# Performance work log

Measured on AMD Instinct MI355X. Metric: run time of the kernel, lower is better.

## Reference

```python
import jax, jax.numpy as jnp
import numpy as np

B, J, D = 1024, 17, 512          # batch, joints, encoder hidden dim
M, K, DT = 34, 2048, 512         # tokens per pose, codebook size, token dim
DDEC, DDEC_I = 32, 64            # decoder hidden dims
L_ENC, L_DEC = 4, 1
DECAY = 0.9
EPS = 1e-5


def _ln(x, g, b):
    m = jnp.mean(x, -1, keepdims=True)
    v = jnp.mean((x - m) ** 2, -1, keepdims=True)
    return (x - m) * jax.lax.rsqrt(v + EPS) * g + b


def _mlp(x, w1, b1, w2, b2):
    return jax.nn.gelu(x @ w1 + b1, approximate=False) @ w2 + b2


def _mixer(x, p, i):
    ln1g, ln1b, tw1, tb1, tw2, tb2, ln2g, ln2b, cw1, cb1, cw2, cb2 = (a[i] for a in p)
    y = jnp.swapaxes(_ln(x, ln1g, ln1b), 1, 2)        # token-mixing over joints
    y = jnp.swapaxes(_mlp(y, tw1, tb1, tw2, tb2), 1, 2)
    z = _mlp(_ln(x + y, ln2g, ln2b), cw1, cb1, cw2, cb2)  # channel-mixing
    return x + y + z


def _forward(joints, invisible_token, start_w, start_b,
             enc_ln1_g, enc_ln1_b, enc_tw1, enc_tb1, enc_tw2, enc_tb2,
             enc_ln2_g, enc_ln2_b, enc_cw1, enc_cb1, enc_cw2, enc_cb2,
             enc_ln_g, enc_ln_b, token_mlp_w, token_mlp_b, feat_w, feat_b,
             dec_ln1_g, dec_ln1_b, dec_tw1, dec_tb1, dec_tw2, dec_tb2,
             dec_ln2_g, dec_ln2_b, dec_cw1, dec_cb1, dec_cw2, dec_cb2,
             dec_token_mlp_w, dec_token_mlp_b, dec_start_w, dec_start_b,
             dec_ln_g, dec_ln_b, rec_w, rec_b,
             codebook, ema_cluster_size, ema_w):
    x = joints[:, :, :2] @ start_w + start_b                  # [B,J,D]
    vis = (joints[:, :, 2:] != 0).astype(x.dtype)             # [B,J,1]
    x = x * vis + invisible_token * (1.0 - vis)
    encp = (enc_ln1_g, enc_ln1_b, enc_tw1, enc_tb1, enc_tw2, enc_tb2,
            enc_ln2_g, enc_ln2_b, enc_cw1, enc_cb1, enc_cw2, enc_cb2)
    for i in range(L_ENC):
        x = _mixer(x, encp, i)
    x = _ln(x, enc_ln_g, enc_ln_b)
    # token_mlp: Linear over joints axis: [B,D,J] -> [B,D,M] -> [B,M,D]
    x = jnp.einsum('bjd,jm->bmd', x, token_mlp_w) + token_mlp_b[None, :, None]
    feat = (x @ feat_w + feat_b).reshape(B * M, DT)           # encode_feat [N,DT]
    # squared euclidean distances to codebook entries
    dists = (jnp.sum(feat * feat, 1, keepdims=True)
             + jnp.sum(codebook * codebook, 1)
             - 2.0 * feat @ codebook.T)                       # [N,K]
    idx = jnp.argmin(dists, axis=1)                           # [N]
    quant = codebook[idx]                                     # == one_hot(idx) @ codebook
    # EMA codebook update (buffers; single-device so all_reduce == identity)
    sg_feat = jax.lax.stop_gradient(feat)
    counts = jax.ops.segment_sum(jnp.ones((B * M,), feat.dtype), idx, num_segments=K)
    dw = jax.ops.segment_sum(sg_feat, idx, num_segments=K)    # == encodings.T @ feat
    cs = ema_cluster_size * DECAY + (1.0 - DECAY) * counts
    n = jnp.sum(cs)
    cs = (cs + 1e-5) / (n + K * 1e-5) * n                     # laplace smoothing
    ema_w_new = ema_w * DECAY + (1.0 - DECAY) * dw
    codebook_new = ema_w_new / cs[:, None]
    e_latent_loss = jnp.mean(jnp.square(jax.lax.stop_gradient(quant) - feat))
    quant = feat + jax.lax.stop_gradient(quant - feat)        # straight-through
    ptf = quant.reshape(B, M, DT)
    out_ptf = jax.lax.stop_gradient(ptf)
    # decoder_token_mlp: Linear over token axis: [B,DT,M] -> [B,DT,J] -> [B,J,DT]
    y = jnp.einsum('bmd,mj->bjd', ptf, dec_token_mlp_w) + dec_token_mlp_b[None, :, None]
    y = y @ dec_start_w + dec_start_b                         # [B,J,DDEC]
    decp = (dec_ln1_g, dec_ln1_b, dec_tw1, dec_tb1, dec_tw2, dec_tb2,
            dec_ln2_g, dec_ln2_b, dec_cw1, dec_cb1, dec_cw2, dec_cb2)
    for i in range(L_DEC):
        y = _mixer(y, decp, i)
    y = _ln(y, dec_ln_g, dec_ln_b)
    rec = y @ rec_w + rec_b                                   # [B,J,2]
    return rec, idx, e_latent_loss, out_ptf, codebook_new


def setup_inputs():
    ks = iter(jax.random.split(jax.random.key(0), 64))
    def nrm(shape, s=0.02):
        return jax.random.normal(next(ks), shape, jnp.float32) * s
    inp = {}
    coords = jax.random.uniform(next(ks), (B, J, 2), jnp.float32)
    inp['joints'] = jnp.concatenate([coords, jnp.ones((B, J, 1), jnp.float32)], -1)
    inp['joints_feature'] = nrm((B, J, 256), 1.0)   # unused (guide_ratio=0)
    inp['cls_logits'] = jnp.zeros((1, 1), jnp.float32)  # unused in tokenizer stage
    inp['invisible_token'] = nrm((1, 1, D))
    inp['start_w'], inp['start_b'] = nrm((2, D)), jnp.zeros((D,), jnp.float32)
    for pre, L, H, HI in (('enc', L_ENC, D, D), ('dec', L_DEC, DDEC, DDEC_I)):
        inp[pre + '_ln1_g'], inp[pre + '_ln1_b'] = jnp.ones((L, H)), jnp.zeros((L, H))
        inp[pre + '_tw1'], inp[pre + '_tb1'] = nrm((L, J, 64)), jnp.zeros((L, 64))
        inp[pre + '_tw2'], inp[pre + '_tb2'] = nrm((L, 64, J)), jnp.zeros((L, J))
        inp[pre + '_ln2_g'], inp[pre + '_ln2_b'] = jnp.ones((L, H)), jnp.zeros((L, H))
        inp[pre + '_cw1'], inp[pre + '_cb1'] = nrm((L, H, HI)), jnp.zeros((L, HI))
        inp[pre + '_cw2'], inp[pre + '_cb2'] = nrm((L, HI, H)), jnp.zeros((L, H))
    inp['enc_ln_g'], inp['enc_ln_b'] = jnp.ones((D,)), jnp.zeros((D,))
    inp['token_mlp_w'], inp['token_mlp_b'] = nrm((J, M)), jnp.zeros((M,))
    inp['feat_w'], inp['feat_b'] = nrm((D, DT)), jnp.zeros((DT,))
    inp['codebook'] = jax.random.normal(next(ks), (K, DT), jnp.float32)
    inp['ema_cluster_size'] = jnp.zeros((K,), jnp.float32)
    inp['ema_w'] = jax.random.normal(next(ks), (K, DT), jnp.float32)
    inp['dec_token_mlp_w'], inp['dec_token_mlp_b'] = nrm((M, J)), jnp.zeros((J,))
    inp['dec_start_w'], inp['dec_start_b'] = nrm((DT, DDEC)), jnp.zeros((DDEC,))
    inp['dec_ln_g'], inp['dec_ln_b'] = jnp.ones((DDEC,)), jnp.zeros((DDEC,))
    inp['rec_w'], inp['rec_b'] = nrm((DDEC, 2)), jnp.zeros((2,))
    return inp


def reference(joints, joints_feature, cls_logits, invisible_token, start_w, start_b,
              enc_ln1_g, enc_ln1_b, enc_tw1, enc_tb1, enc_tw2, enc_tb2,
              enc_ln2_g, enc_ln2_b, enc_cw1, enc_cb1, enc_cw2, enc_cb2,
              enc_ln_g, enc_ln_b, token_mlp_w, token_mlp_b, feat_w, feat_b,
              codebook, ema_cluster_size, ema_w,
              dec_ln1_g, dec_ln1_b, dec_tw1, dec_tb1, dec_tw2, dec_tb2,
              dec_ln2_g, dec_ln2_b, dec_cw1, dec_cb1, dec_cw2, dec_cb2,
              dec_token_mlp_w, dec_token_mlp_b, dec_start_w, dec_start_b,
              dec_ln_g, dec_ln_b, rec_w, rec_b):
    # joints_feature / cls_logits unused: guide_ratio=0, stage_pct='tokenizer'
    return _forward(joints, invisible_token, start_w, start_b,
                    enc_ln1_g, enc_ln1_b, enc_tw1, enc_tb1, enc_tw2, enc_tb2,
                    enc_ln2_g, enc_ln2_b, enc_cw1, enc_cb1, enc_cw2, enc_cb2,
                    enc_ln_g, enc_ln_b, token_mlp_w, token_mlp_b, feat_w, feat_b,
                    dec_ln1_g, dec_ln1_b, dec_tw1, dec_tb1, dec_tw2, dec_tb2,
                    dec_ln2_g, dec_ln2_b, dec_cw1, dec_cb1, dec_cw2, dec_cb2,
                    dec_token_mlp_w, dec_token_mlp_b, dec_start_w, dec_start_b,
                    dec_ln_g, dec_ln_b, rec_w, rec_b,
                    codebook, ema_cluster_size, ema_w)
```

## Files before the change

### kernel.cpp

```cpp
#include <hip/hip_runtime.h>
#include <math.h>

constexpr int Bn = 1024, Jn = 17, Mn = 34;
constexpr int RJ = Bn * Jn;
constexpr int RM = Bn * Mn;
constexpr size_t SZX = (size_t)RJ * 512;
constexpr size_t SZM = (size_t)RM * 512;

typedef __attribute__((ext_vector_type(8))) short bf16x8;
typedef __attribute__((ext_vector_type(4))) float f32x4;
typedef unsigned long long u64;
typedef unsigned short u16;
typedef unsigned int u32;

__device__ __forceinline__ float gelu_f(float x) {
  return 0.5f * x * (1.0f + erff(x * 0.7071067811865475f));
}
__device__ __forceinline__ u16 bf16_rne(float x) {
  u32 u = __float_as_uint(x);
  u += 0x7fffu + ((u >> 16) & 1u);
  return (u16)(u >> 16);
}
__device__ __forceinline__ float bf16_f(u16 h) {
  return __uint_as_float((u32)h << 16);
}

typedef __attribute__((address_space(1))) const void gas_t;
typedef __attribute__((address_space(3))) void las_t;
__device__ __forceinline__ void gll16(const void* g, void* l) {
  __builtin_amdgcn_global_load_lds((gas_t*)g, (las_t*)l, 16, 0, 0);
}

__global__ __launch_bounds__(256) void embed_kernel(
    const float* __restrict__ joints, const float* __restrict__ inv,
    const float* __restrict__ sw, const float* __restrict__ sb,
    float* __restrict__ out) {
  int tid = blockIdx.x * 256 + threadIdx.x;
  int row = tid >> 9, d = tid & 511;
  float j0 = joints[row * 3 + 0];
  float j1 = joints[row * 3 + 1];
  float j2 = joints[row * 3 + 2];
  float x = fmaf(j0, sw[d], fmaf(j1, sw[512 + d], sb[d]));
  float v = (j2 != 0.0f) ? 1.0f : 0.0f;
  out[tid] = x * v + inv[d] * (1.0f - v);
}

__global__ __launch_bounds__(256) void mixer_fused(
    const float* __restrict__ x_in, float* __restrict__ res_out,
    u16* __restrict__ oh, u16* __restrict__ ol,
    const float* __restrict__ g1, const float* __restrict__ b1,
    const float* __restrict__ tw1, const float* __restrict__ tb1,
    const float* __restrict__ tw2, const float* __restrict__ tb2,
    const float* __restrict__ g2, const float* __restrict__ b2,
    const float* __restrict__ W1, const float* __restrict__ W2,
    u16* __restrict__ Th1, u16* __restrict__ Tl1,
    u16* __restrict__ Th2, u16* __restrict__ Tl2) {
  __shared__ float xs[17][512];
  __shared__ float sw1[17 * 64], sw2[64 * 17], sb1v[64], sb2v[17];
  __shared__ float stats[17][2];
  const int tid = threadIdx.x;
  const int b = blockIdx.x;
  {
    int gid = b * 256 + tid;
    int k = gid >> 9, n = gid & 511;
    float v = W1[gid];
    u16 h = bf16_rne(v);
    Th1[(size_t)n * 512 + k] = h;
    Tl1[(size_t)n * 512 + k] = bf16_rne(v - bf16_f(h));
    v = W2[gid];
    h = bf16_rne(v);
    Th2[(size_t)n * 512 + k] = h;
    Tl2[(size_t)n * 512 + k] = bf16_rne(v - bf16_f(h));
  }
  for (int i = tid; i < 17 * 64; i += 256) { sw1[i] = tw1[i]; sw2[i] = tw2[i]; }
  if (tid < 64) sb1v[tid] = tb1[tid];
  if (tid < 17) sb2v[tid] = tb2[tid];
  const float* px = x_in + (size_t)b * 17 * 512;
  for (int i = tid; i < 17 * 512; i += 256) xs[i >> 9][i & 511] = px[i];
  __syncthreads();
  const int wv = tid >> 6, ln_ = tid & 63;
  for (int j = wv; j < 17; j += 4) {
    float v[8];
    float s = 0.0f;
#pragma unroll
    for (int i = 0; i < 8; i++) { v[i] = xs[j][ln_ + 64 * i]; s += v[i]; }
#pragma unroll
    for (int m = 32; m; m >>= 1) s += __shfl_xor(s, m);
    float mean = s * (1.0f / 512.0f);
    float s2 = 0.0f;
#pragma unroll
    for (int i = 0; i < 8; i++) { float t = v[i] - mean; s2 += t * t; }
#pragma unroll
    for (int m = 32; m; m >>= 1) s2 += __shfl_xor(s2, m);
    float rs = 1.0f / sqrtf(s2 * (1.0f / 512.0f) + 1e-5f);
    if (ln_ == 0) { stats[j][0] = mean; stats[j][1] = rs; }
  }
  __syncthreads();
  for (int cc = 0; cc < 2; cc++) {
    int d = tid + cc * 256;
    float gd = g1[d], bd = b1[d];
    float t[17], acc[17];
#pragma unroll
    for (int j = 0; j < 17; j++) {
      t[j] = (xs[j][d] - stats[j][0]) * stats[j][1] * gd + bd;
      acc[j] = 0.0f;
    }
    for (int k = 0; k < 64; k++) {
      float h = sb1v[k];
#pragma unroll
      for (int j = 0; j < 17; j++) h = fmaf(t[j], sw1[j * 64 + k], h);
      h = gelu_f(h);
#pragma unroll
      for (int j = 0; j < 17; j++) acc[j] = fmaf(h, sw2[k * 17 + j], acc[j]);
    }
#pragma unroll
    for (int j = 0; j < 17; j++) {
      float r = xs[j][d] + acc[j] + sb2v[j];
      xs[j][d] = r;
      res_out[((size_t)b * 17 + j) * 512 + d] = r;
    }
  }
  __syncthreads();
  for (int j = wv; j < 17; j += 4) {
    float v[8];
    float s = 0.0f;
#pragma unroll
    for (int i = 0; i < 8; i++) { v[i] = xs[j][ln_ + 64 * i]; s += v[i]; }
#pragma unroll
    for (int m = 32; m; m >>= 1) s += __shfl_xor(s, m);
    float mean = s * (1.0f / 512.0f);
    float s2 = 0.0f;
#pragma unroll
    for (int i = 0; i < 8; i++) { float t = v[i] - mean; s2 += t * t; }
#pragma unroll
    for (int m = 32; m; m >>= 1) s2 += __shfl_xor(s2, m);
    float rs = 1.0f / sqrtf(s2 * (1.0f / 512.0f) + 1e-5f);
#pragma unroll
    for (int i = 0; i < 8; i++) {
      int d = ln_ + 64 * i;
      float o = (v[i] - mean) * rs * g2[d] + b2[d];
      u16 h = bf16_rne(o);
      size_t off = ((size_t)b * 17 + j) * 512 + d;
      oh[off] = h;
      ol[off] = bf16_rne(o - bf16_f(h));
    }
  }
}

__global__ __launch_bounds__(256) void lnmix_fused(
    const float* __restrict__ x_in, u16* __restrict__ oh, u16* __restrict__ ol,
    const float* __restrict__ g, const float* __restrict__ bb,
    const float* __restrict__ w, const float* __restrict__ bias,
    const float* __restrict__ Wf, u16* __restrict__ Thf, u16* __restrict__ Tlf) {
  __shared__ float xs[17][513];
  __shared__ float sw[17 * 34], sb[34];
  const int tid = threadIdx.x;
  const int b = blockIdx.x;
  {
    int gid = b * 256 + tid;
    int k = gid >> 9, n = gid & 511;
    float v = Wf[gid];
    u16 h = bf16_rne(v);
    Thf[(size_t)n * 512 + k] = h;
    Tlf[(size_t)n * 512 + k] = bf16_rne(v - bf16_f(h));
  }
  for (int i = tid; i < 17 * 34; i += 256) sw[i] = w[i];
  if (tid < 34) sb[tid] = bias[tid];
  const float* px = x_in + (size_t)b * 17 * 512;
  for (int i = tid; i < 17 * 512; i += 256) xs[i >> 9][i & 511] = px[i];
  __syncthreads();
  const int wv = tid >> 6, ln_ = tid & 63;
  for (int j = wv; j < 17; j += 4) {
    float v[8];
    float s = 0.0f;
#pragma unroll
    for (int i = 0; i < 8; i++) { v[i] = xs[j][ln_ + 64 * i]; s += v[i]; }
#pragma unroll
    for (int m = 32; m; m >>= 1) s += __shfl_xor(s, m);
    float mean = s * (1.0f / 512.0f);
    float s2 = 0.0f;
#pragma unroll
    for (int i = 0; i < 8; i++) { float t = v[i] - mean; s2 += t * t; }
#pragma unroll
    for (int m = 32; m; m >>= 1) s2 += __shfl_xor(s2, m);
    float rs = 1.0f / sqrtf(s2 * (1.0f / 512.0f) + 1e-5f);
#pragma unroll
    for (int i = 0; i < 8; i++) {
      int d = ln_ + 64 * i;
      xs[j][d] = (v[i] - mean) * rs * g[d] + bb[d];
    }
  }
  __syncthreads();
  for (int cc = 0; cc < 2; cc++) {
    int d = tid + cc * 256;
    float t[17];
#pragma unroll
    for (int j = 0; j < 17; j++) t[j] = xs[j][d];
#pragma unroll
    for (int m = 0; m < 34; m++) {
      float s = sb[m];
#pragma unroll
      for (int j = 0; j < 17; j++) s = fmaf(t[j], sw[j * 34 + m], s);
      size_t o = ((size_t)b * 34 + m) * 512 + d;
      u16 h = bf16_rne(s);
      oh[o] = h;
      ol[o] = bf16_rne(s - bf16_f(h));
    }
  }
}

__global__ __launch_bounds__(256) void splitnorm_kernel(
    const float* __restrict__ CBm, u16* __restrict__ hi, u16* __restrict__ lo,
    float* __restrict__ cnorm, u64* __restrict__ packed, int* __restrict__ cnt) {
  int gid = blockIdx.x * 256 + threadIdx.x;
  for (int i = gid; i < RM; i += 131072) packed[i] = ~0ull;
  if (gid < 2048) cnt[gid] = 0;
  int wave = threadIdx.x >> 6, lane = threadIdx.x & 63;
  int k = blockIdx.x * 4 + wave;
  const float4* p4 = (const float4*)(CBm + (size_t)k * 512);
  ushort4* h4 = (ushort4*)(hi + (size_t)k * 512);
  ushort4* l4 = (ushort4*)(lo + (size_t)k * 512);
  float s = 0.0f;
#pragma unroll
  for (int i = 0; i < 2; i++) {
    float4 x = p4[lane + 64 * i];
    ushort4 h, l;
    h.x = bf16_rne(x.x); l.x = bf16_rne(x.x - bf16_f(h.x));
    h.y = bf16_rne(x.y); l.y = bf16_rne(x.y - bf16_f(h.y));
    h.z = bf16_rne(x.z); l.z = bf16_rne(x.z - bf16_f(h.z));
    h.w = bf16_rne(x.w); l.w = bf16_rne(x.w - bf16_f(h.w));
    h4[lane + 64 * i] = h;
    l4[lane + 64 * i] = l;
    s = fmaf(x.x, x.x, s); s = fmaf(x.y, x.y, s);
    s = fmaf(x.z, x.z, s); s = fmaf(x.w, x.w, s);
  }
#pragma unroll
  for (int m = 32; m; m >>= 1) s += __shfl_xor(s, m);
  if (lane == 0) cnorm[k] = s;
}

template <int GELU_FLAG, int RES_FLAG, int HILO_OUT>
__global__ __launch_bounds__(256, 4) void mgemm64(
    const u16* __restrict__ Ah, const u16* __restrict__ Al,
    const u16* __restrict__ Bh, const u16* __restrict__ Bl,
    const float* __restrict__ bias, const float* __restrict__ R,
    float* __restrict__ C, u16* __restrict__ Oh, u16* __restrict__ Ol, int N) {
  __shared__ __align__(16) u16 sAh[2048], sAl[2048], sBh[4096], sBl[4096];
  const int tid = threadIdx.x;
  const int m0 = blockIdx.x * 64, n0 = blockIdx.y * 128;
  const int lane = tid & 63, wave = tid >> 6;
  const int wm = wave >> 1, wn = wave & 1;
  const int fr = lane & 15, q = lane >> 4;
  const int ra = tid >> 2, ca = (tid & 3) ^ ((ra >> 1) & 3);
  const size_t aoff = (size_t)(m0 + ra) * 512 + ca * 8;
  const int rb0 = tid >> 2, cb0 = (tid & 3) ^ ((rb0 >> 1) & 3);
  const int ci1 = tid + 256;
  const int rb1 = ci1 >> 2, cb1 = (ci1 & 3) ^ ((rb1 >> 1) & 3);
  const size_t boff0 = (size_t)(n0 + rb0) * 512 + cb0 * 8;
  const size_t boff1 = (size_t)(n0 + rb1) * 512 + cb1 * 8;
  const int ldA = wave * 512;
  const int ldB0 = wave * 512, ldB1 = 2048 + wave * 512;
  int fca[2], fcb[4];
#pragma unroll
  for (int mt = 0; mt < 2; mt++) {
    int rra = wm * 32 + mt * 16 + fr;
    fca[mt] = (rra * 4 + (q ^ ((rra >> 1) & 3))) * 8;
  }
#pragma unroll
  for (int nt = 0; nt < 4; nt++) {
    int rrb = wn * 64 + nt * 16 + fr;
    fcb[nt] = (rrb * 4 + (q ^ ((rrb >> 1) & 3))) * 8;
  }
  f32x4 acc[2][4];
#pragma unroll
  for (int i = 0; i < 2; i++)
#pragma unroll
    for (int j = 0; j < 4; j++) {
      acc[i][j][0] = 0.0f; acc[i][j][1] = 0.0f;
      acc[i][j][2] = 0.0f; acc[i][j][3] = 0.0f;
    }
  for (int k0 = 0; k0 < 512; k0 += 32) {
    gll16(Ah + aoff + k0, &sAh[ldA]);
    gll16(Al + aoff + k0, &sAl[ldA]);
    gll16(Bh + boff0 + k0, &sBh[ldB0]);
    gll16(Bh + boff1 + k0, &sBh[ldB1]);
    gll16(Bl + boff0 + k0, &sBl[ldB0]);
    gll16(Bl + boff1 + k0, &sBl[ldB1]);
    __syncthreads();
    bf16x8 fah[2], fal[2], fbh[4], fbl[4];
#pragma unroll
    for (int mt = 0; mt < 2; mt++) {
      fah[mt] = *(const bf16x8*)&sAh[fca[mt]];
      fal[mt] = *(const bf16x8*)&sAl[fca[mt]];
    }
#pragma unroll
    for (int nt = 0; nt < 4; nt++) {
      fbh[nt] = *(const bf16x8*)&sBh[fcb[nt]];
      fbl[nt] = *(const bf16x8*)&sBl[fcb[nt]];
    }
#pragma unroll
    for (int mt = 0; mt < 2; mt++)
#pragma unroll
      for (int nt = 0; nt < 4; nt++) {
        acc[mt][nt] = __builtin_amdgcn_mfma_f32_16x16x32_bf16(
            fah[mt], fbh[nt], acc[mt][nt], 0, 0, 0);
        acc[mt][nt] = __builtin_amdgcn_mfma_f32_16x16x32_bf16(
            fah[mt], fbl[nt], acc[mt][nt], 0, 0, 0);
        acc[mt][nt] = __builtin_amdgcn_mfma_f32_16x16x32_bf16(
            fal[mt], fbh[nt], acc[mt][nt], 0, 0, 0);
      }
    __syncthreads();
  }
#pragma unroll
  for (int mt = 0; mt < 2; mt++)
#pragma unroll
    for (int reg = 0; reg < 4; reg++) {
      int row = m0 + wm * 32 + mt * 16 + q * 4 + reg;
#pragma unroll
      for (int nt = 0; nt < 4; nt++) {
        int col = n0 + wn * 64 + nt * 16 + fr;
        float v = acc[mt][nt][reg] + bias[col];
        if (GELU_FLAG) v = gelu_f(v);
        if (RES_FLAG) v += R[(size_t)row * N + col];
        if (HILO_OUT) {
          u16 h = bf16_rne(v);
          Oh[(size_t)row * N + col] = h;
          Ol[(size_t)row * N + col] = bf16_rne(v - bf16_f(h));
        } else {
          C[(size_t)row * N + col] = v;
        }
      }
    }
}

#define MG_PROLOGUE()                                                        \
  const int tid = threadIdx.x;                                               \
  const int m0 = blockIdx.x * 128, n0 = blockIdx.y * 128;                    \
  const int lane = tid & 63, wave = tid >> 6;                                \
  const int wm = wave >> 1, wn = wave & 1;                                   \
  const int fr = lane & 15, q = lane >> 4, qd = q;                           \
  const int ci0 = wave * 128 + lane, ci1 = ci0 + 64;                         \
  const int r0 = ci0 >> 2, c0x = (ci0 & 3) ^ ((r0 >> 1) & 3);                \
  const int r1 = ci1 >> 2, c1x = (ci1 & 3) ^ ((r1 >> 1) & 3);                \
  const size_t aoff0 = (size_t)(m0 + r0) * 512 + c0x * 8;                    \
  const size_t aoff1 = (size_t)(m0 + r1) * 512 + c1x * 8;                    \
  const size_t boff0 = (size_t)(n0 + r0) * 512 + c0x * 8;                    \
  const size_t boff1 = (size_t)(n0 + r1) * 512 + c1x * 8;                    \
  const int ld0 = wave * 1024, ld1 = ld0 + 512;       \
  int fca[4], fcb[4];                                                        \
  _Pragma("unroll") for (int t4 = 0; t4 < 4; t4++) {                         \
    int rra = wm * 64 + t4 * 16 + fr;                                        \
    int rrb = wn * 64 + t4 * 16 + fr;                                        \
    int sz = q ^ ((fr >> 1) & 3);                                            \
    fca[t4] = (rra * 4 + sz) * 8;                                            \
    fcb[t4] = (rrb * 4 + sz) * 8;                                            \
  }                                                                          \
  f32x4 acc[4][4];                                                           \
  _Pragma("unroll") for (int i = 0; i < 4; i++)                              \
    _Pragma("unroll") for (int j = 0; j < 4; j++) {                          \
      acc[i][j][0] = 0.0f; acc[i][j][1] = 0.0f;                              \
      acc[i][j][2] = 0.0f; acc[i][j][3] = 0.0f;                              \
    }

#define MG_KLOOP(Ah, Al, Bh, Bl)                                             \
  for (int k0 = 0; k0 < 512; k0 += 32) {                                     \
    gll16(Ah + aoff0 + k0, &sAh[ld0]);                                       \
    gll16(Ah + aoff1 + k0, &sAh[ld1]);                                       \
    gll16(Al + aoff0 + k0, &sAl[ld0]);                                       \
    gll16(Al + aoff1 + k0, &sAl[ld1]);                                       \
    gll16(Bh + boff0 + k0, &sBh[ld0]);                                       \
    gll16(Bh + boff1 + k0, &sBh[ld1]);                                       \
    gll16(Bl + boff0 + k0, &sBl[ld0]);                                       \
    gll16(Bl + boff1 + k0, &sBl[ld1]);                                       \
    __syncthreads();                                                         \
    bf16x8 fah[4], fal[4], fbh[4], fbl[4];                                   \
    _Pragma("unroll") for (int t4 = 0; t4 < 4; t4++) {                       \
      fah[t4] = *(const bf16x8*)&sAh[fca[t4]];                               \
      fal[t4] = *(const bf16x8*)&sAl[fca[t4]];                               \
      fbh[t4] = *(const bf16x8*)&sBh[fcb[t4]];                               \
      fbl[t4] = *(const bf16x8*)&sBl[fcb[t4]];                               \
    }                                                                        \
    _Pragma("unroll") for (int mt = 0; mt < 4; mt++)                         \
      _Pragma("unroll") for (int nt = 0; nt < 4; nt++) {                     \
        acc[mt][nt] = __builtin_amdgcn_mfma_f32_16x16x32_bf16(               \
            fah[mt], fbh[nt], acc[mt][nt], 0, 0, 0);                         \
        acc[mt][nt] = __builtin_amdgcn_mfma_f32_16x16x32_bf16(               \
            fah[mt], fbl[nt], acc[mt][nt], 0, 0, 0);                         \
        acc[mt][nt] = __builtin_amdgcn_mfma_f32_16x16x32_bf16(               \
            fal[mt], fbh[nt], acc[mt][nt], 0, 0, 0);                         \
      }                                                                      \
    __syncthreads();                                                         \
  }

__global__ __launch_bounds__(256, 4) void dist_mfma(
    const u16* __restrict__ Ah, const u16* __restrict__ Al,
    const u16* __restrict__ Bh, const u16* __restrict__ Bl,
    const float* __restrict__ cnorm, u64* __restrict__ packed) {
  __shared__ __align__(16) u16 sAh[4096], sAl[4096], sBh[4096], sBl[4096];
  MG_PROLOGUE()
  MG_KLOOP(Ah, Al, Bh, Bl)
#pragma unroll
  for (int mt = 0; mt < 4; mt++)
#pragma unroll
    for (int reg = 0; reg < 4; reg++) {
      u64 best = ~0ull;
#pragma unroll
      for (int nt = 0; nt < 4; nt++) {
        int c = n0 + wn * 64 + nt * 16 + fr;
        float d = cnorm[c] - 2.0f * acc[mt][nt][reg];
        u32 ub = __float_as_uint(d);
        ub = (ub & 0x80000000u) ? ~ub : (ub | 0x80000000u);
        u64 p = ((u64)ub << 32) | (u32)c;
        best = (p < best) ? p : best;
      }
#pragma unroll
      for (int mm = 1; mm <= 8; mm <<= 1) {
        u32 h2 = __shfl_xor((u32)(best >> 32), mm);
        u32 l2 = __shfl_xor((u32)best, mm);
        u64 o = ((u64)h2 << 32) | l2;
        best = (o < best) ? o : best;
      }
      if (fr == 0) {
        int row = m0 + wm * 64 + mt * 16 + qd * 4 + reg;
        atomicMin(&packed[row], best);
      }
    }
}

__global__ __launch_bounds__(256) void idxcount_kernel(
    const u64* __restrict__ packed, float* __restrict__ o_idx,
    int* __restrict__ cnt) {
  __shared__ int h[2048];
  for (int i = threadIdx.x; i < 2048; i += 256) h[i] = 0;
  __syncthreads();
  int r = blockIdx.x * 256 + threadIdx.x;
  u32 k = (u32)packed[r];
  o_idx[r] = (float)k;
  atomicAdd(&h[k], 1);
  __syncthreads();
  for (int i = threadIdx.x; i < 2048; i += 256) {
    int v = h[i];
    if (v) atomicAdd(&cnt[i], v);
  }
}

__global__ __launch_bounds__(256) void scan_kernel(
    const int* __restrict__ cnt, int* __restrict__ base,
    int* __restrict__ cursor, const float* __restrict__ ema_cs,
    float* __restrict__ nbuf) {
  __shared__ int part[256];
  __shared__ float esum[256];
  int t = threadIdx.x;
  int local[8];
  int s = 0;
  float es = 0.0f;
#pragma unroll
  for (int i = 0; i < 8; i++) {
    local[i] = cnt[t * 8 + i];
    s += local[i];
    es += ema_cs[t * 8 + i];
  }
  part[t] = s;
  esum[t] = es;
  __syncthreads();
  for (int off = 1; off < 256; off <<= 1) {
    int v = (t >= off) ? part[t - off] : 0;
    __syncthreads();
    part[t] += v;
    __syncthreads();
  }
  int run = part[t] - s;
#pragma unroll
  for (int i = 0; i < 8; i++) {
    base[t * 8 + i] = run;
    cursor[t * 8 + i] = run;
    run += local[i];
  }
  for (int o = 128; o; o >>= 1) {
    if (t < o) esum[t] += esum[t + o];
    __syncthreads();
  }
  if (t == 0) nbuf[0] = 0.9f * esum[0] + 0.1f * (float)RM;
}

__global__ __launch_bounds__(256) void scatter_kernel(
    const u64* __restrict__ packed, int* __restrict__ cursor,
    u32* __restrict__ bucket, float* __restrict__ dw) {
  __shared__ int h[2048];
  __shared__ int gb[2048];
  int gid = blockIdx.x * 256 + threadIdx.x;
  for (int i = gid; i < 2048 * 512; i += RM) dw[i] = 0.0f;
  for (int i = threadIdx.x; i < 2048; i += 256) h[i] = 0;
  __syncthreads();
  int k = (int)(u32)packed[gid];
  int lrank = atomicAdd(&h[k], 1);
  __syncthreads();
  for (int i = threadIdx.x; i < 2048; i += 256) {
    int v = h[i];
    gb[i] = v ? atomicAdd(&cursor[i], v) : 0;
  }
  __syncthreads();
  bucket[gb[k] + lrank] = ((u32)k << 17) | (u32)gid;
}

__global__ __launch_bounds__(256) void quant_out_kernel(
    const u16* __restrict__ fh, const u16* __restrict__ fl,
    const float* __restrict__ CBm, const u64* __restrict__ packed,
    float* __restrict__ ptf_out, float* __restrict__ lpart) {
  __shared__ float wred[4];
  int row = blockIdx.x * 2 + (threadIdx.x >> 7);
  int t = threadIdx.x & 127;
  int k = (int)(u32)packed[row];
  uint2 hb = ((const uint2*)(fh + (size_t)row * 512))[t];
  uint2 lb = ((const uint2*)(fl + (size_t)row * 512))[t];
  float f0 = bf16_f((u16)hb.x) + bf16_f((u16)lb.x);
  float f1 = bf16_f((u16)(hb.x >> 16)) + bf16_f((u16)(lb.x >> 16));
  float f2 = bf16_f((u16)hb.y) + bf16_f((u16)lb.y);
  float f3 = bf16_f((u16)(hb.y >> 16)) + bf16_f((u16)(lb.y >> 16));
  float4 c = ((const float4*)(CBm + (size_t)k * 512))[t];
  float* po = ptf_out + (size_t)row * 512 + 4 * t;
  po[0] = c.x; po[1] = c.y; po[2] = c.z; po[3] = c.w;
  float dx = c.x - f0, dy = c.y - f1, dz = c.z - f2, dwv = c.w - f3;
  float ls = dx * dx + dy * dy + dz * dz + dwv * dwv;
#pragma unroll
  for (int m = 32; m; m >>= 1) ls += __shfl_xor(ls, m);
  if ((threadIdx.x & 63) == 0) wred[threadIdx.x >> 6] = ls;
  __syncthreads();
  if (threadIdx.x == 0)
    lpart[blockIdx.x] = wred[0] + wred[1] + wred[2] + wred[3];
}

__global__ __launch_bounds__(256) void dwsum_chunk_kernel(
    const u16* __restrict__ fh, const u16* __restrict__ fl,
    const u32* __restrict__ bucket, float* __restrict__ dw) {
  __shared__ u32 sp[64];
  const int t = threadIdx.x;
  if (t < 64) sp[t] = bucket[blockIdx.x * 64 + t];
  __syncthreads();
  float ax = 0.0f, ay = 0.0f;
  int curk = (int)(sp[0] >> 17);
  u32 hb = *(const u32*)(fh + (size_t)(sp[0] & 0x1FFFF) * 512 + 2 * t);
  u32 lb = *(const u32*)(fl + (size_t)(sp[0] & 0x1FFFF) * 512 + 2 * t);
  for (int i = 0; i < 64; i++) {
    u32 hn = 0, ln2 = 0;
    if (i + 1 < 64) {
      hn = *(const u32*)(fh + (size_t)(sp[i + 1] & 0x1FFFF) * 512 + 2 * t);
      ln2 = *(const u32*)(fl + (size_t)(sp[i + 1] & 0x1FFFF) * 512 + 2 * t);
    }
    int k = (int)(sp[i] >> 17);
    if (k != curk) {
      atomicAdd(&dw[(size_t)curk * 512 + 2 * t], ax);
      atomicAdd(&dw[(size_t)curk * 512 + 2 * t + 1], ay);
      ax = 0.0f; ay = 0.0f; curk = k;
    }
    ax += bf16_f((u16)hb) + bf16_f((u16)lb);
    ay += bf16_f((u16)(hb >> 16)) + bf16_f((u16)(lb >> 16));
    hb = hn; lb = ln2;
  }
  atomicAdd(&dw[(size_t)curk * 512 + 2 * t], ax);
  atomicAdd(&dw[(size_t)curk * 512 + 2 * t + 1], ay);
}

__global__ __launch_bounds__(256) void cbnew_kernel(
    const float* __restrict__ ema_w, const float* __restrict__ dw,
    const float* __restrict__ ema_cs, const int* __restrict__ cnt,
    const float* __restrict__ nbuf, float* __restrict__ outp,
    const float* __restrict__ lpart, float* __restrict__ loss_out) {
  int tid = blockIdx.x * 256 + threadIdx.x;
  int k = tid >> 9;
  float n = nbuf[0];
  float cs = ema_cs[k] * 0.9f + 0.1f * (float)cnt[k];
  cs = (cs + 1e-5f) / (n + 0.02048f) * n;
  outp[tid] = (ema_w[tid] * 0.9f + 0.1f * dw[tid]) / cs;
  if (blockIdx.x == 0) {
    __shared__ float red[256];
    float s = 0.0f;
    for (int i = threadIdx.x; i < RM / 2; i += 256) s += lpart[i];
    red[threadIdx.x] = s;
    __syncthreads();
    for (int o = 128; o; o >>= 1) {
      if (threadIdx.x < o) red[threadIdx.x] += red[threadIdx.x + o];
      __syncthreads();
    }
    if (threadIdx.x == 0)
      loss_out[0] = red[0] / (float)((size_t)RM * 512);
  }
}

__global__ __launch_bounds__(256) void decoder_fused(
    const float* __restrict__ ptf,
    const float* __restrict__ dtokw, const float* __restrict__ dtokb,
    const float* __restrict__ dsw, const float* __restrict__ dsb,
    const float* __restrict__ ln1g, const float* __restrict__ ln1b,
    const float* __restrict__ tw1, const float* __restrict__ tb1,
    const float* __restrict__ tw2, const float* __restrict__ tb2,
    const float* __restrict__ ln2g, const float* __restrict__ ln2b,
    const float* __restrict__ cw1, const float* __restrict__ cb1,
    const float* __restrict__ cw2, const float* __restrict__ cb2,
    const float* __restrict__ lng, const float* __restrict__ lnb,
    const float* __restrict__ recw, const float* __restrict__ recb,
    float* __restrict__ o_rec) {
  __shared__ float buf[34 * 257];
  __shared__ float yS[17][257];
  __shared__ float zS[17][33];
  __shared__ float t2S[17][33];
  __shared__ float hS[17][65];
  __shared__ float sdw[34 * 17];
  __shared__ float stw1[17 * 64], stw2[64 * 17];
  const int tid = threadIdx.x;
  const int b = blockIdx.x;
  for (int i = tid; i < 34 * 17; i += 256) sdw[i] = dtokw[i];
  for (int i = tid; i < 17 * 64; i += 256) { stw1[i] = tw1[i]; stw2[i] = tw2[i]; }
  float zacc0 = 0.0f, zacc1 = 0.0f, zacc2 = 0.0f;
  const int j0 = tid >> 5, dd0 = tid & 31;
  const int p1 = tid + 256;
  const int j1 = p1 >> 5, dd1 = p1 & 31;
  const int p2 = tid + 512;
  const int j2 = p2 >> 5, dd2 = p2 & 31;
  for (int ch = 0; ch < 2; ch++) {
    for (int m = 0; m < 34; m++)
      buf[m * 257 + tid] = ptf[((size_t)b * 34 + m) * 512 + ch * 256 + tid];
    __syncthreads();
#pragma unroll 1
    for (int j = 0; j < 17; j++) {
      float s = dtokb[j];
#pragma unroll
      for (int m = 0; m < 34; m++) s = fmaf(buf[m * 257 + tid], sdw[m * 17 + j], s);
      yS[j][tid] = s;
    }
    __syncthreads();
    for (int i = tid; i < 256 * 32; i += 256) {
      int d = i >> 5, dd = i & 31;
      buf[d * 33 + dd] = dsw[(size_t)(ch * 256 + d) * 32 + dd];
    }
    __syncthreads();
    {
      float s = 0.0f;
      for (int d = 0; d < 256; d++) s = fmaf(yS[j0][d], buf[d * 33 + dd0], s);
      zacc0 += s;
      float s1 = 0.0f;
      for (int d = 0; d < 256; d++) s1 = fmaf(yS[j1][d], buf[d * 33 + dd1], s1);
      zacc1 += s1;
      if (tid < 32) {
        float s2 = 0.0f;
        for (int d = 0; d < 256; d++) s2 = fmaf(yS[j2][d], buf[d * 33 + dd2], s2);
        zacc2 += s2;
      }
    }
    __syncthreads();
  }
  zS[j0][dd0] = zacc0 + dsb[dd0];
  zS[j1][dd1] = zacc1 + dsb[dd1];
  if (tid < 32) zS[j2][dd2] = zacc2 + dsb[dd2];
  __syncthreads();
  if (tid < 17) {
    float m = 0.0f;
#pragma unroll
    for (int d = 0; d < 32; d++) m += zS[tid][d];
    m *= (1.0f / 32.0f);
    float v = 0.0f;
#pragma unroll
    for (int d = 0; d < 32; d++) { float t = zS[tid][d] - m; v += t * t; }
    float rs = 1.0f / sqrtf(v * (1.0f / 32.0f) + 1e-5f);
#pragma unroll
    for (int d = 0; d < 32; d++)
      t2S[tid][d] = (zS[tid][d] - m) * rs * ln1g[d] + ln1b[d];
  }
  __syncthreads();
  if (tid < 32) {
    float t[17], acc[17];
#pragma unroll
    for (int j = 0; j < 17; j++) { t[j] = t2S[j][tid]; acc[j] = 0.0f; }
    for (int k = 0; k < 64; k++) {
      float h = tb1[k];
#pragma unroll
      for (int j = 0; j < 17; j++) h = fmaf(t[j], stw1[j * 64 + k], h);
      h = gelu_f(h);
#pragma unroll
      for (int j = 0; j < 17; j++) acc[j] = fmaf(h, stw2[k * 17 + j], acc[j]);
    }
#pragma unroll
    for (int j = 0; j < 17; j++) zS[j][tid] = zS[j][tid] + acc[j] + tb2[j];
  }
  __syncthreads();
  if (tid < 17) {
    float m = 0.0f;
#pragma unroll
    for (int d = 0; d < 32; d++) m += zS[tid][d];
    m *= (1.0f / 32.0f);
    float v = 0.0f;
#pragma unroll
    for (int d = 0; d < 32; d++) { float t = zS[tid][d] - m; v += t * t; }
    float rs = 1.0f / sqrtf(v * (1.0f / 32.0f) + 1e-5f);
#pragma unroll
    for (int d = 0; d < 32; d++)
      t2S[tid][d] = (zS[tid][d] - m) * rs * ln2g[d] + ln2b[d];
  }
  __syncthreads();
  for (int p = tid; p < 17 * 64; p += 256) {
    int j = p >> 6, k = p & 63;
    float s = cb1[k];
#pragma unroll
    for (int d = 0; d < 32; d++) s = fmaf(t2S[j][d], cw1[d * 64 + k], s);
    hS[j][k] = gelu_f(s);
  }
  __syncthreads();
  {
    float s = cb2[dd0];
#pragma unroll
    for (int k = 0; k < 64; k++) s = fmaf(hS[j0][k], cw2[k * 32 + dd0], s);
    zS[j0][dd0] += s;
    float s1 = cb2[dd1];
#pragma unroll
    for (int k = 0; k < 64; k++) s1 = fmaf(hS[j1][k], cw2[k * 32 + dd1], s1);
    zS[j1][dd1] += s1;
    if (tid < 32) {
      float s2 = cb2[dd2];
#pragma unroll
      for (int k = 0; k < 64; k++) s2 = fmaf(hS[j2][k], cw2[k * 32 + dd2], s2);
      zS[j2][dd2] += s2;
    }
  }
  __syncthreads();
  if (tid < 17) {
    float m = 0.0f;
#pragma unroll
    for (int d = 0; d < 32; d++) m += zS[tid][d];
    m *= (1.0f / 32.0f);
    float v = 0.0f;
#pragma unroll
    for (int d = 0; d < 32; d++) { float t = zS[tid][d] - m; v += t * t; }
    float rs = 1.0f / sqrtf(v * (1.0f / 32.0f) + 1e-5f);
#pragma unroll
    for (int d = 0; d < 32; d++)
      t2S[tid][d] = (zS[tid][d] - m) * rs * lng[d] + lnb[d];
  }
  __syncthreads();
  if (tid < 34) {
    int j = tid >> 1, c = tid & 1;
    float s = recb[c];
#pragma unroll
    for (int d = 0; d < 32; d++) s = fmaf(t2S[j][d], recw[d * 2 + c], s);
    o_rec[((size_t)b * 17 + j) * 2 + c] = s;
  }
}

extern "C" void kernel_launch(void* const* d_in, const int* in_sizes, int n_in,
                              void* d_out, int out_size, void* d_ws, size_t ws_size,
                              hipStream_t stream) {
  const float* joints   = (const float*)d_in[0];
  const float* inv_tok  = (const float*)d_in[3];
  const float* start_w  = (const float*)d_in[4];
  const float* start_b  = (const float*)d_in[5];
  const float* e_ln1g = (const float*)d_in[6];
  const float* e_ln1b = (const float*)d_in[7];
  const float* e_tw1  = (const float*)d_in[8];
  const float* e_tb1  = (const float*)d_in[9];
  const float* e_tw2  = (const float*)d_in[10];
  const float* e_tb2  = (const float*)d_in[11];
  const float* e_ln2g = (const float*)d_in[12];
  const float* e_ln2b = (const float*)d_in[13];
  const float* e_cw1  = (const float*)d_in[14];
  const float* e_cb1  = (const float*)d_in[15];
  const float* e_cw2  = (const float*)d_in[16];
  const float* e_cb2  = (const float*)d_in[17];
  const float* d_ln1g = (const float*)d_in[18];
  const float* d_ln1b = (const float*)d_in[19];
  const float* d_tw1  = (const float*)d_in[20];
  const float* d_tb1  = (const float*)d_in[21];
  const float* d_tw2  = (const float*)d_in[22];
  const float* d_tb2  = (const float*)d_in[23];
  const float* d_ln2g = (const float*)d_in[24];
  const float* d_ln2b = (const float*)d_in[25];
  const float* d_cw1  = (const float*)d_in[26];
  const float* d_cb1  = (const float*)d_in[27];
  const float* d_cw2  = (const float*)d_in[28];
  const float* d_cb2  = (const float*)d_in[29];
  const float* enc_lng = (const float*)d_in[30];
  const float* enc_lnb = (const float*)d_in[31];
  const float* tok_w   = (const float*)d_in[32];
  const float* tok_b   = (const float*)d_in[33];
  const float* feat_w  = (const float*)d_in[34];
  const float* feat_b  = (const float*)d_in[35];
  const float* codebook = (const float*)d_in[36];
  const float* ema_cs   = (const float*)d_in[37];
  const float* ema_w    = (const float*)d_in[38];
  const float* dtok_w   = (const float*)d_in[39];
  const float* dtok_b   = (const float*)d_in[40];
  const float* dstart_w = (const float*)d_in[41];
  const float* dstart_b = (const float*)d_in[42];
  const float* dec_lng  = (const float*)d_in[43];
  const float* dec_lnb  = (const float*)d_in[44];
  const float* rec_w    = (const float*)d_in[45];
  const float* rec_b    = (const float*)d_in[46];

  float* ws = (float*)d_ws;
  float* Ab  = ws;
  float* Bb  = ws + SZX;
  float* Cc  = ws + 2 * SZX;
  float* P1e = ws + 3 * SZX;
  float* P2e = ws + 4 * SZX;
  float* cbs = ws + 5 * SZX;
  float* cnorm = cbs + 1048576;
  u64*  packed = (u64*)(cnorm + 2048);
  int*  cnt    = (int*)(cnorm + 2048 + 69632);
  int*  basebuf = cnt + 2048;
  int*  cursor  = basebuf + 2048;
  u32*  bucket  = (u32*)(cursor + 2048);
  float* lpart  = (float*)(bucket + RM);
  float* nbuf   = lpart + RM / 2;
  float* dw     = nbuf + 2048;
  u16* WTh1 = (u16*)dw;
  u16* WTl1 = (u16*)(dw + 131072);
  u16* WTh2 = (u16*)(dw + 262144);
  u16* WTl2 = (u16*)(dw + 393216);
  u16* P1eh = (u16*)P1e;  u16* P1el = (u16*)(P1e + SZX / 2);
  u16* P2eh = (u16*)P2e;  u16* P2el = (u16*)(P2e + SZX / 2);
  u16* P1mh = (u16*)Ab;   u16* P1ml = (u16*)Bb;
  u16* P2mh = (u16*)Cc;   u16* P2ml = (u16*)P1e;
  u16* chh = (u16*)cbs;   u16* cll = (u16*)(cbs + 524288);

  float* outp = (float*)d_out;
  float* o_rec = outp;
  float* o_idx = outp + (size_t)RJ * 2;
  float* o_loss = o_idx + RM;
  float* o_ptf = o_loss + 1;
  float* o_cb = o_ptf + SZM;

  embed_kernel<<<(RJ * 512) / 256, 256, 0, stream>>>(joints, inv_tok, start_w, start_b, Ab);
  for (int i = 0; i < 4; i++) {
    mixer_fused<<<Bn, 256, 0, stream>>>(
        Ab, Bb, P1eh, P1el,
        e_ln1g + i * 512, e_ln1b + i * 512,
        e_tw1 + i * 17 * 64, e_tb1 + i * 64, e_tw2 + i * 64 * 17, e_tb2 + i * 17,
        e_ln2g + i * 512, e_ln2b + i * 512,
        e_cw1 + (size_t)i * 512 * 512, e_cw2 + (size_t)i * 512 * 512,
        WTh1, WTl1, WTh2, WTl2);
    mgemm64<1, 0, 1><<<dim3(RJ / 64, 4), 256, 0, stream>>>(
        P1eh, P1el, WTh1, WTl1, e_cb1 + i * 512, nullptr, nullptr, P2eh, P2el, 512);
    mgemm64<0, 1, 0><<<dim3(RJ / 64, 4), 256, 0, stream>>>(
        P2eh, P2el, WTh2, WTl2, e_cb2 + i * 512, Bb, Ab, nullptr, nullptr, 512);
  }
  lnmix_fused<<<Bn, 256, 0, stream>>>(Ab, P1mh, P1ml, enc_lng, enc_lnb, tok_w, tok_b,
                                      feat_w, WTh1, WTl1);
  mgemm64<0, 0, 1><<<dim3(RM / 64, 4), 256, 0, stream>>>(
      P1mh, P1ml, WTh1, WTl1, feat_b, nullptr, nullptr, P2mh, P2ml, 512);

  splitnorm_kernel<<<2048 / 4, 256, 0, stream>>>(codebook, chh, cll, cnorm, packed, cnt);
  dist_mfma<<<dim3(RM / 128, 2048 / 128), 256, 0, stream>>>(P2mh, P2ml, chh, cll, cnorm, packed);

  idxcount_kernel<<<RM / 256, 256, 0, stream>>>(packed, o_idx, cnt);
  scan_kernel<<<1, 256, 0, stream>>>(cnt, basebuf, cursor, ema_cs, nbuf);
  scatter_kernel<<<RM / 256, 256, 0, stream>>>(packed, cursor, bucket, dw);
  quant_out_kernel<<<RM / 2, 256, 0, stream>>>(P2mh, P2ml, codebook, packed, o_ptf, lpart);
  dwsum_chunk_kernel<<<RM / 64, 256, 0, stream>>>(P2mh, P2ml, bucket, dw);
  cbnew_kernel<<<(2048 * 512) / 256, 256, 0, stream>>>(
      ema_w, dw, ema_cs, cnt, nbuf, o_cb, lpart, o_loss);

  decoder_fused<<<Bn, 256, 0, stream>>>(
      o_ptf, dtok_w, dtok_b, dstart_w, dstart_b,
      d_ln1g, d_ln1b, d_tw1, d_tb1, d_tw2, d_tb2, d_ln2g, d_ln2b,
      d_cw1, d_cb1, d_cw2, d_cb2, dec_lng, dec_lnb, rec_w, rec_b, o_rec);
}
```

Before: 1.616 ms.

## Read small weights directly from global and register-block two columns per thread

```diff
diff --git a/kernel.cpp b/kernel.cpp
--- a/kernel.cpp
+++ b/kernel.cpp
@@ -56,7 +56,6 @@
     u16* __restrict__ Th1, u16* __restrict__ Tl1,
     u16* __restrict__ Th2, u16* __restrict__ Tl2) {
   __shared__ float xs[17][512];
-  __shared__ float sw1[17 * 64], sw2[64 * 17], sb1v[64], sb2v[17];
   __shared__ float stats[17][2];
   const int tid = threadIdx.x;
   const int b = blockIdx.x;
@@ -72,9 +71,6 @@
     Th2[(size_t)n * 512 + k] = h;
     Tl2[(size_t)n * 512 + k] = bf16_rne(v - bf16_f(h));
   }
-  for (int i = tid; i < 17 * 64; i += 256) { sw1[i] = tw1[i]; sw2[i] = tw2[i]; }
-  if (tid < 64) sb1v[tid] = tb1[tid];
-  if (tid < 17) sb2v[tid] = tb2[tid];
   const float* px = x_in + (size_t)b * 17 * 512;
   for (int i = tid; i < 17 * 512; i += 256) xs[i >> 9][i & 511] = px[i];
   __syncthreads();
@@ -96,28 +92,45 @@
     if (ln_ == 0) { stats[j][0] = mean; stats[j][1] = rs; }
   }
   __syncthreads();
-  for (int cc = 0; cc < 2; cc++) {
-    int d = tid + cc * 256;
-    float gd = g1[d], bd = b1[d];
-    float t[17], acc[17];
+  {
+    const int d0 = tid, d1 = tid + 256;
+    float ga = g1[d0], ba = b1[d0];
+    float gb = g1[d1], bb2 = b1[d1];
+    float t0[17], t1[17], a0[17], a1[17];
 #pragma unroll
     for (int j = 0; j < 17; j++) {
-      t[j] = (xs[j][d] - stats[j][0]) * stats[j][1] * gd + bd;
-      acc[j] = 0.0f;
-    }
+      float mj = stats[j][0], rj = stats[j][1];
+      t0[j] = (xs[j][d0] - mj) * rj * ga + ba;
+      t1[j] = (xs[j][d1] - mj) * rj * gb + bb2;
+      a0[j] = 0.0f; a1[j] = 0.0f;
+    }
+#pragma unroll 1
     for (int k = 0; k < 64; k++) {
-      float h = sb1v[k];
-#pragma unroll
-      for (int j = 0; j < 17; j++) h = fmaf(t[j], sw1[j * 64 + k], h);
-      h = gelu_f(h);
-#pragma unroll
-      for (int j = 0; j < 17; j++) acc[j] = fmaf(h, sw2[k * 17 + j], acc[j]);
+      float h0 = tb1[k], h1 = h0;
+#pragma unroll
+      for (int j = 0; j < 17; j++) {
+        float w = tw1[j * 64 + k];
+        h0 = fmaf(t0[j], w, h0);
+        h1 = fmaf(t1[j], w, h1);
+      }
+      h0 = gelu_f(h0);
+      h1 = gelu_f(h1);
+#pragma unroll
+      for (int j = 0; j < 17; j++) {
+        float w = tw2[k * 17 + j];
+        a0[j] = fmaf(h0, w, a0[j]);
+        a1[j] = fmaf(h1, w, a1[j]);
+      }
     }
 #pragma unroll
     for (int j = 0; j < 17; j++) {
-      float r = xs[j][d] + acc[j] + sb2v[j];
-      xs[j][d] = r;
-      res_out[((size_t)b * 17 + j) * 512 + d] = r;
+      float tb = tb2[j];
+      float r0 = xs[j][d0] + a0[j] + tb;
+      float r1 = xs[j][d1] + a1[j] + tb;
+      xs[j][d0] = r0;
+      xs[j][d1] = r1;
+      res_out[((size_t)b * 17 + j) * 512 + d0] = r0;
+      res_out[((size_t)b * 17 + j) * 512 + d1] = r1;
     }
   }
   __syncthreads();
@@ -153,7 +166,6 @@
     const float* __restrict__ w, const float* __restrict__ bias,
     const float* __restrict__ Wf, u16* __restrict__ Thf, u16* __restrict__ Tlf) {
   __shared__ float xs[17][513];
-  __shared__ float sw[17 * 34], sb[34];
   const int tid = threadIdx.x;
   const int b = blockIdx.x;
   {
@@ -164,8 +176,6 @@
     Thf[(size_t)n * 512 + k] = h;
     Tlf[(size_t)n * 512 + k] = bf16_rne(v - bf16_f(h));
   }
-  for (int i = tid; i < 17 * 34; i += 256) sw[i] = w[i];
-  if (tid < 34) sb[tid] = bias[tid];
   const float* px = x_in + (size_t)b * 17 * 512;
   for (int i = tid; i < 17 * 512; i += 256) xs[i >> 9][i & 511] = px[i];
   __syncthreads();
@@ -191,20 +201,28 @@
     }
   }
   __syncthreads();
-  for (int cc = 0; cc < 2; cc++) {
-    int d = tid + cc * 256;
-    float t[17];
-#pragma unroll
-    for (int j = 0; j < 17; j++) t[j] = xs[j][d];
-#pragma unroll
+  {
+    const int d0 = tid, d1 = tid + 256;
+    float t0[17], t1[17];
+#pragma unroll
+    for (int j = 0; j < 17; j++) { t0[j] = xs[j][d0]; t1[j] = xs[j][d1]; }
+#pragma unroll 1
     for (int m = 0; m < 34; m++) {
-      float s = sb[m];
-#pragma unroll
-      for (int j = 0; j < 17; j++) s = fmaf(t[j], sw[j * 34 + m], s);
-      size_t o = ((size_t)b * 34 + m) * 512 + d;
-      u16 h = bf16_rne(s);
-      oh[o] = h;
-      ol[o] = bf16_rne(s - bf16_f(h));
+      float s0 = bias[m], s1 = s0;
+#pragma unroll
+      for (int j = 0; j < 17; j++) {
+        float wv2 = w[j * 34 + m];
+        s0 = fmaf(t0[j], wv2, s0);
+        s1 = fmaf(t1[j], wv2, s1);
+      }
+      size_t o0 = ((size_t)b * 34 + m) * 512 + d0;
+      u16 h0 = bf16_rne(s0);
+      oh[o0] = h0;
+      ol[o0] = bf16_rne(s0 - bf16_f(h0));
+      size_t o1 = o0 + 256;
+      u16 h1 = bf16_rne(s1);
+      oh[o1] = h1;
+      ol[o1] = bf16_rne(s1 - bf16_f(h1));
     }
   }
 }
@@ -600,58 +618,65 @@
     const float* __restrict__ lng, const float* __restrict__ lnb,
     const float* __restrict__ recw, const float* __restrict__ recb,
     float* __restrict__ o_rec) {
-  __shared__ float buf[34 * 257];
-  __shared__ float yS[17][257];
+  __shared__ float yS[17][260];
   __shared__ float zS[17][33];
   __shared__ float t2S[17][33];
   __shared__ float hS[17][65];
-  __shared__ float sdw[34 * 17];
-  __shared__ float stw1[17 * 64], stw2[64 * 17];
   const int tid = threadIdx.x;
   const int b = blockIdx.x;
-  for (int i = tid; i < 34 * 17; i += 256) sdw[i] = dtokw[i];
-  for (int i = tid; i < 17 * 64; i += 256) { stw1[i] = tw1[i]; stw2[i] = tw2[i]; }
   float zacc0 = 0.0f, zacc1 = 0.0f, zacc2 = 0.0f;
   const int j0 = tid >> 5, dd0 = tid & 31;
-  const int p1 = tid + 256;
-  const int j1 = p1 >> 5, dd1 = p1 & 31;
-  const int p2 = tid + 512;
-  const int j2 = p2 >> 5, dd2 = p2 & 31;
+  const int j1 = (tid + 256) >> 5;
+  const int j2 = (tid + 512) >> 5;
   for (int ch = 0; ch < 2; ch++) {
+    float p[34];
+#pragma unroll
     for (int m = 0; m < 34; m++)
-      buf[m * 257 + tid] = ptf[((size_t)b * 34 + m) * 512 + ch * 256 + tid];
-    __syncthreads();
+      p[m] = ptf[((size_t)b * 34 + m) * 512 + ch * 256 + tid];
 #pragma unroll 1
     for (int j = 0; j < 17; j++) {
       float s = dtokb[j];
 #pragma unroll
-      for (int m = 0; m < 34; m++) s = fmaf(buf[m * 257 + tid], sdw[m * 17 + j], s);
+      for (int m = 0; m < 34; m++) s = fmaf(p[m], dtokw[m * 17 + j], s);
       yS[j][tid] = s;
-    }
-    __syncthreads();
-    for (int i = tid; i < 256 * 32; i += 256) {
-      int d = i >> 5, dd = i & 31;
-      buf[d * 33 + dd] = dsw[(size_t)(ch * 256 + d) * 32 + dd];
     }
     __syncthreads();
     {
-      float s = 0.0f;
-      for (int d = 0; d < 256; d++) s = fmaf(yS[j0][d], buf[d * 33 + dd0], s);
-      zacc0 += s;
-      float s1 = 0.0f;
-      for (int d = 0; d < 256; d++) s1 = fmaf(yS[j1][d], buf[d * 33 + dd1], s1);
-      zacc1 += s1;
+      const float4* y0 = (const float4*)&yS[j0][0];
+      const float4* y1 = (const float4*)&yS[j1][0];
+      const float* wg = dsw + (size_t)ch * 256 * 32 + dd0;
+#pragma unroll 1
+      for (int d4 = 0; d4 < 64; d4++) {
+        float4 va = y0[d4];
+        float4 vb = y1[d4];
+        float w0 = wg[(4 * d4 + 0) * 32];
+        float w1 = wg[(4 * d4 + 1) * 32];
+        float w2 = wg[(4 * d4 + 2) * 32];
+        float w3 = wg[(4 * d4 + 3) * 32];
+        zacc0 = fmaf(va.x, w0, zacc0); zacc0 = fmaf(va.y, w1, zacc0);
+        zacc0 = fmaf(va.z, w2, zacc0); zacc0 = fmaf(va.w, w3, zacc0);
+        zacc1 = fmaf(vb.x, w0, zacc1); zacc1 = fmaf(vb.y, w1, zacc1);
+        zacc1 = fmaf(vb.z, w2, zacc1); zacc1 = fmaf(vb.w, w3, zacc1);
+      }
       if (tid < 32) {
-        float s2 = 0.0f;
-        for (int d = 0; d < 256; d++) s2 = fmaf(yS[j2][d], buf[d * 33 + dd2], s2);
-        zacc2 += s2;
+        const float4* y2 = (const float4*)&yS[j2][0];
+#pragma unroll 1
+        for (int d4 = 0; d4 < 64; d4++) {
+          float4 vc = y2[d4];
+          float w0 = wg[(4 * d4 + 0) * 32];
+          float w1 = wg[(4 * d4 + 1) * 32];
+          float w2 = wg[(4 * d4 + 2) * 32];
+          float w3 = wg[(4 * d4 + 3) * 32];
+          zacc2 = fmaf(vc.x, w0, zacc2); zacc2 = fmaf(vc.y, w1, zacc2);
+          zacc2 = fmaf(vc.z, w2, zacc2); zacc2 = fmaf(vc.w, w3, zacc2);
+        }
       }
     }
     __syncthreads();
   }
   zS[j0][dd0] = zacc0 + dsb[dd0];
-  zS[j1][dd1] = zacc1 + dsb[dd1];
-  if (tid < 32) zS[j2][dd2] = zacc2 + dsb[dd2];
+  zS[j1][dd0] = zacc1 + dsb[dd0];
+  if (tid < 32) zS[j2][dd0] = zacc2 + dsb[dd0];
   __syncthreads();
   if (tid < 17) {
     float m = 0.0f;
@@ -674,10 +699,10 @@
     for (int k = 0; k < 64; k++) {
       float h = tb1[k];
 #pragma unroll
-      for (int j = 0; j < 17; j++) h = fmaf(t[j], stw1[j * 64 + k], h);
+      for (int j = 0; j < 17; j++) h = fmaf(t[j], tw1[j * 64 + k], h);
       h = gelu_f(h);
 #pragma unroll
-      for (int j = 0; j < 17; j++) acc[j] = fmaf(h, stw2[k * 17 + j], acc[j]);
+      for (int j = 0; j < 17; j++) acc[j] = fmaf(h, tw2[k * 17 + j], acc[j]);
     }
 #pragma unroll
     for (int j = 0; j < 17; j++) zS[j][tid] = zS[j][tid] + acc[j] + tb2[j];
@@ -706,19 +731,21 @@
   }
   __syncthreads();
   {
-    float s = cb2[dd0];
-#pragma unroll
-    for (int k = 0; k < 64; k++) s = fmaf(hS[j0][k], cw2[k * 32 + dd0], s);
-    zS[j0][dd0] += s;
-    float s1 = cb2[dd1];
-#pragma unroll
-    for (int k = 0; k < 64; k++) s1 = fmaf(hS[j1][k], cw2[k * 32 + dd1], s1);
-    zS[j1][dd1] += s1;
+    float cb = cb2[dd0];
+    float s0 = cb, s1 = cb;
+#pragma unroll
+    for (int k = 0; k < 64; k++) {
+      float w = cw2[k * 32 + dd0];
+      s0 = fmaf(hS[j0][k], w, s0);
+      s1 = fmaf(hS[j1][k], w, s1);
+    }
+    zS[j0][dd0] += s0;
+    zS[j1][dd0] += s1;
     if (tid < 32) {
-      float s2 = cb2[dd2];
-#pragma unroll
-      for (int k = 0; k < 64; k++) s2 = fmaf(hS[j2][k], cw2[k * 32 + dd2], s2);
-      zS[j2][dd2] += s2;
+      float s2 = cb;
+#pragma unroll
+      for (int k = 0; k < 64; k++) s2 = fmaf(hS[j2][k], cw2[k * 32 + dd0], s2);
+      zS[j2][dd0] += s2;
     }
   }
   __syncthreads();
```

Measured after the change: 1.361 ms. 1.19x faster.
